# Kernel tuning notes

Hardware: AMD Instinct MI355X
Metric: run time of the kernel (lower is better)

The kernel has to match this reference:

```python
import jax, jax.numpy as jnp
import numpy as np

DIM = 2048
H = 16       # num_heads
HKV = 4      # num_kv_heads
HD = DIM // H  # head_dim = 128
REP = H // HKV
ROPE_BASE = 10000.0
QK_GAIN_INIT = 1.0
B, T = 4, 2048


def rms_norm(x):
    # F.rms_norm with eps=None -> machine eps of dtype, no weight
    eps = jnp.finfo(x.dtype).eps
    return x * jax.lax.rsqrt(jnp.mean(x * x, axis=-1, keepdims=True) + eps)


def apply_rotary_emb(x, cos, sin):
    # x: [B, h, T, HD]; cos/sin: [T, HD//2]
    h = x.shape[-1] // 2
    x1, x2 = x[..., :h], x[..., h:]
    return jnp.concatenate((x1 * cos + x2 * sin, -x1 * sin + x2 * cos), axis=-1)


def setup_inputs() -> dict:
    key = jax.random.key(0)
    ks = jax.random.split(key, 6)
    kv_dim = HKV * HD
    x = jax.random.normal(ks[0], (B, T, DIM), dtype=jnp.float32)
    Wq = jax.random.normal(ks[1], (DIM, DIM), dtype=jnp.float32) * 0.02
    Wk = jax.random.normal(ks[2], (kv_dim, DIM), dtype=jnp.float32) * 0.02
    Wv = jax.random.normal(ks[3], (kv_dim, DIM), dtype=jnp.float32) * 0.02
    Wproj = jax.random.normal(ks[4], (DIM, DIM), dtype=jnp.float32) * 0.02
    q_gain = jnp.full((H,), QK_GAIN_INIT, dtype=jnp.float32)
    return {"x": x, "Wq": Wq, "Wk": Wk, "Wv": Wv, "Wproj": Wproj, "q_gain": q_gain}


def reference(x, Wq, Wk, Wv, Wproj, q_gain):
    Bs, Ts, D = x.shape
    # QKV projections (bias-free Linear: x @ W.T)
    q = (x @ Wq.T).reshape(Bs, Ts, H, HD).transpose(0, 2, 1, 3)      # [B,H,T,HD]
    k = (x @ Wk.T).reshape(Bs, Ts, HKV, HD).transpose(0, 2, 1, 3)    # [B,HKV,T,HD]
    v = (x @ Wv.T).reshape(Bs, Ts, HKV, HD).transpose(0, 2, 1, 3)
    # RMSNorm over head_dim
    q, k = rms_norm(q), rms_norm(k)
    # rotary
    inv_freq = 1.0 / (ROPE_BASE ** (jnp.arange(0, HD, 2, dtype=jnp.float32) / HD))
    t = jnp.arange(Ts, dtype=jnp.float32)
    freqs = jnp.outer(t, inv_freq)  # [T, HD//2]
    cos, sin = jnp.cos(freqs), jnp.sin(freqs)
    q = apply_rotary_emb(q, cos, sin)
    k = apply_rotary_emb(k, cos, sin)
    # per-head query gain
    q = q * q_gain[None, :, None, None]
    # GQA attention without materializing repeated K/V
    qg = q.reshape(Bs, HKV, REP, Ts, HD)
    scale = 1.0 / jnp.sqrt(jnp.asarray(HD, dtype=q.dtype))
    scores = jnp.einsum('bgrtd,bgsd->bgrts', qg, k) * scale  # [B,HKV,REP,T,T]
    causal = jnp.tril(jnp.ones((Ts, Ts), dtype=bool))
    scores = jnp.where(causal, scores, jnp.finfo(scores.dtype).min)
    attn = jax.nn.softmax(scores, axis=-1)
    y = jnp.einsum('bgrts,bgsd->bgrtd', attn, v)              # [B,HKV,REP,T,HD]
    y = y.reshape(Bs, H, Ts, HD).transpose(0, 2, 1, 3).reshape(Bs, Ts, D)
    return y @ Wproj.T
```

## Files before the change

### kernel.cpp

```cpp
#include <hip/hip_runtime.h>
#include <stdint.h>

typedef unsigned short u16;
typedef __attribute__((ext_vector_type(4))) float f32x4;
typedef __attribute__((ext_vector_type(8))) __bf16 bf16x8;
typedef __attribute__((ext_vector_type(4))) u16 u16x4;
typedef __attribute__((ext_vector_type(8))) u16 u16x8;

#define T_SEQ 2048
#define NB 4
#define NH 16
#define NKV 4
#define HDIM 128
#define PSTR 72

__device__ __forceinline__ u16 f2bf(float f) {
  __bf16 h = (__bf16)f;
  return __builtin_bit_cast(u16, h);
}
__device__ __forceinline__ float bf2f(u16 u) {
  union { uint32_t u; float f; } v; v.u = ((uint32_t)u) << 16;
  return v.f;
}
__device__ __forceinline__ void gload16(const void* g, void* l) {
  __builtin_amdgcn_global_load_lds((const __attribute__((address_space(1))) void*)g,
                                   (__attribute__((address_space(3))) void*)l, 16, 0, 0);
}
__device__ __forceinline__ f32x4 mfma16(bf16x8 a, bf16x8 b, f32x4 c) {
  return __builtin_amdgcn_mfma_f32_16x16x32_bf16(a, b, c, 0, 0, 0);
}

__global__ __launch_bounds__(256) void cvt_bf16(const float* __restrict__ in,
                                                u16* __restrict__ out, int n) {
  int idx = blockIdx.x * 256 + threadIdx.x;
  int stride = gridDim.x * 256;
  for (int i = idx * 4; i < n; i += stride * 4) {
    f32x4 v = *(const f32x4*)(in + i);
    u16x4 o;
    o[0] = f2bf(v[0]); o[1] = f2bf(v[1]); o[2] = f2bf(v[2]); o[3] = f2bf(v[3]);
    *(u16x4*)(out + i) = o;
  }
}

template <int MODE>
__global__ __launch_bounds__(512, 2) void gemm256(const u16* __restrict__ A,
                                                  const u16* __restrict__ Bt,
                                                  u16* __restrict__ q_o, u16* __restrict__ k_o,
                                                  u16* __restrict__ v_o, float* __restrict__ f_o,
                                                  int K, int ntn, int cpx) {
  __shared__ __align__(16) u16 As[2][256 * 64];
  __shared__ __align__(16) u16 Bs[2][256 * 64];
  const int tid = threadIdx.x;
  const int l = tid & 63, w = tid >> 6;
  const int l16 = l & 15, g16 = l >> 4;
  const int wr = w >> 2, wc = w & 3;

  const int oid = blockIdx.x;
  const int wid = (oid & 7) * cpx + (oid >> 3);
  const int m0 = (wid / ntn) * 256, n0 = (wid % ntn) * 256;

  f32x4 acc[8][4] = {};

  const int srow = tid >> 3, scc = tid & 7;
  const u16* pA[4];
  const u16* pB[4];
#pragma unroll
  for (int j = 0; j < 4; ++j) {
    int row = j * 64 + srow;
    int cc = scc ^ (row & 7);
    pA[j] = A + (size_t)(m0 + row) * K + cc * 8;
    pB[j] = Bt + (size_t)(n0 + row) * K + cc * 8;
  }

#define STAGE(buf)                                              \
  {                                                             \
    char* ab = (char*)As[buf] + w * 1024;                       \
    char* bb = (char*)Bs[buf] + w * 1024;                       \
    _Pragma("unroll")                                           \
    for (int j = 0; j < 4; ++j) {                               \
      gload16(pA[j], ab + j * 8192);                            \
      pA[j] += 64;                                              \
    }                                                           \
    _Pragma("unroll")                                           \
    for (int j = 0; j < 4; ++j) {                               \
      gload16(pB[j], bb + j * 8192);                            \
      pB[j] += 64;                                              \
    }                                                           \
  }

  const int ntk = K >> 6;
  STAGE(0);
  __syncthreads();

  for (int t = 0; t < ntk; ++t) {
    const int buf = t & 1;
    if (t + 1 < ntk) STAGE(buf ^ 1);
#pragma unroll
    for (int ks = 0; ks < 2; ++ks) {
      bf16x8 bfr[4];
#pragma unroll
      for (int nf = 0; nf < 4; ++nf) {
        int brow = wc * 64 + nf * 16 + l16;
        int slot = (ks * 4 + g16) ^ (brow & 7);
        bfr[nf] = *(const bf16x8*)&Bs[buf][brow * 64 + slot * 8];
      }
#pragma unroll
      for (int rh = 0; rh < 2; ++rh) {
        bf16x8 af[4];
#pragma unroll
        for (int f = 0; f < 4; ++f) {
          int arow = wr * 128 + rh * 64 + f * 16 + l16;
          int slot = (ks * 4 + g16) ^ (arow & 7);
          af[f] = *(const bf16x8*)&As[buf][arow * 64 + slot * 8];
        }
        __builtin_amdgcn_s_setprio(1);
#pragma unroll
        for (int f = 0; f < 4; ++f)
#pragma unroll
          for (int nf = 0; nf < 4; ++nf)
            acc[rh * 4 + f][nf] = mfma16(af[f], bfr[nf], acc[rh * 4 + f][nf]);
        __builtin_amdgcn_s_setprio(0);
      }
    }
    __syncthreads();
  }
#undef STAGE

#pragma unroll
  for (int rf = 0; rf < 8; ++rf) {
#pragma unroll
    for (int rr = 0; rr < 4; ++rr) {
      int row = m0 + wr * 128 + rf * 16 + g16 * 4 + rr;
#pragma unroll
      for (int nf = 0; nf < 4; ++nf) {
        int n = n0 + wc * 64 + nf * 16 + l16;
        float val = acc[rf][nf][rr];
        if (MODE == 1) {
          f_o[(size_t)row * 2048 + n] = val;
        } else {
          int b = row >> 11, t = row & (T_SEQ - 1);
          u16 bv = f2bf(val);
          if (n < 2048) {
            int h = n >> 7, d = n & 127;
            q_o[((size_t)(b * NH + h) * T_SEQ + t) * HDIM + d] = bv;
          } else if (n < 2560) {
            int n2 = n - 2048; int h = n2 >> 7, d = n2 & 127;
            k_o[((size_t)(b * NKV + h) * T_SEQ + t) * HDIM + d] = bv;
          } else {
            int n2 = n - 2560; int h = n2 >> 7, d = n2 & 127;
            v_o[((size_t)(b * NKV + h) * T_SEQ + t) * HDIM + d] = bv;
          }
        }
      }
    }
  }
}

__global__ __launch_bounds__(256) void rmsrope(u16* __restrict__ buf,
                                               const float* __restrict__ gains,
                                               int nheads, float fold, int useGain) {
  const int w = threadIdx.x >> 6, l = threadIdx.x & 63;
  const int rid = blockIdx.x * 4 + w;
  const int t = rid & (T_SEQ - 1);
  const int h = (rid >> 11) % nheads;
  u16* p = buf + (size_t)rid * HDIM;
  float x1 = bf2f(p[l]), x2 = bf2f(p[l + 64]);
  float ss = x1 * x1 + x2 * x2;
#pragma unroll
  for (int m = 32; m; m >>= 1) ss += __shfl_xor(ss, m, 64);
  float rn = rsqrtf(ss * (1.0f / 128.0f) + 1.1920928955078125e-7f);
  float g = useGain ? gains[h] * fold : fold;
  float sc = rn * g;
  float inv = exp2f(-(float)l * (13.287712379549449f / 64.0f));
  float ang = (float)t * inv;
  float s, c;
  __sincosf(ang, &s, &c);
  float o1 = (x1 * c + x2 * s) * sc;
  float o2 = (x2 * c - x1 * s) * sc;
  p[l] = f2bf(o1);
  p[l + 64] = f2bf(o2);
}

__global__ __launch_bounds__(256) void vtrans(const u16* __restrict__ in,
                                              u16* __restrict__ out) {
  __shared__ u16 tileT[64][PSTR];
  const int tid = threadIdx.x;
  const int t0 = blockIdx.x * 64, d0 = blockIdx.y * 64, bg = blockIdx.z;
  const int row = tid >> 2, c0 = (tid & 3) * 16;
  const u16* src = in + ((size_t)bg * T_SEQ + t0 + row) * HDIM + d0 + c0;
  u16x8 a = *(const u16x8*)src;
  u16x8 bb = *(const u16x8*)(src + 8);
#pragma unroll
  for (int j = 0; j < 8; ++j) {
    tileT[c0 + j][row] = a[j];
    tileT[c0 + 8 + j][row] = bb[j];
  }
  __syncthreads();
  u16* dst = out + ((size_t)bg * HDIM + d0 + row) * T_SEQ + t0 + c0;
  *(u16x8*)dst = *(const u16x8*)&tileT[row][c0];
  *(u16x8*)(dst + 8) = *(const u16x8*)&tileT[row][c0 + 8];
}

__global__ __launch_bounds__(256) void attn_fwd3(const u16* __restrict__ qb,
                                                 const u16* __restrict__ kb,
                                                 const u16* __restrict__ vtb,
                                                 u16* __restrict__ yb,
                                                 const float* __restrict__ gains) {
  __shared__ __align__(16) u16 Ks[64 * 128];
  __shared__ __align__(16) u16 Vs[128 * 64];
  __shared__ __align__(16) u16 Ps[4][32 * PSTR];

  const int tid = threadIdx.x, l = tid & 63, w = tid >> 6;
  const int l16 = l & 15, g16 = l >> 4;

  const int oid = blockIdx.x + 8 * blockIdx.y;
  const int wid = (oid & 7) * 64 + (oid >> 3);
  const int pair = wid & 7, bh = wid >> 3;
  const int b = bh >> 4, h = bh & 15, gr = h >> 2;

  const float Mh = 16.33f * fabsf(gains[h]) + 0.5f;
  const u16* kbase = kb + (size_t)(b * NKV + gr) * T_SEQ * HDIM;
  const u16* vtbase = vtb + (size_t)(b * NKV + gr) * HDIM * T_SEQ;

  for (int phase = 0; phase < 2; ++phase) {
    const int qt = phase ? (15 - pair) : pair;
    const int q0 = qt * 128 + w * 32;
    const int qhi = q0 + 31;

    bf16x8 qf[2][4];
    const u16* qbase = qb + ((size_t)bh * T_SEQ + q0) * HDIM;
#pragma unroll
    for (int nf = 0; nf < 2; ++nf)
#pragma unroll
      for (int s = 0; s < 4; ++s)
        qf[nf][s] = *(const bf16x8*)(qbase + (size_t)(nf * 16 + l16) * HDIM + s * 32 + g16 * 8);

    f32x4 oacc[2][8] = {};
    float den[2] = {0.f, 0.f};
    const int ntile = 2 * qt + 2;

    for (int kt = 0; kt < ntile; ++kt) {
#pragma unroll
      for (int r = 0; r < 4; ++r) {
        int c = r * 256 + tid;
        int row = c >> 4, c16 = c & 15;
        int sc = c16 ^ (row & 7);
        gload16(kbase + ((size_t)(kt * 64 + row)) * HDIM + sc * 8,
                (char*)Ks + (r * 256 + w * 64) * 16);
      }
#pragma unroll
      for (int r = 0; r < 4; ++r) {
        int c = r * 256 + tid;
        int row = c >> 3, c8 = c & 7;
        int sc = c8 ^ (row & 7);
        gload16(vtbase + (size_t)row * T_SEQ + kt * 64 + sc * 8,
                (char*)Vs + (r * 256 + w * 64) * 16);
      }
      __syncthreads();

      if (kt * 64 <= qhi) {
        f32x4 sacc[4][2] = {};
        __builtin_amdgcn_s_setprio(1);
#pragma unroll
        for (int mt = 0; mt < 4; ++mt) {
          int key = mt * 16 + l16;
#pragma unroll
          for (int s = 0; s < 4; ++s) {
            bf16x8 kf = *(const bf16x8*)&Ks[key * 128 + ((s * 4 + g16) ^ (key & 7)) * 8];
#pragma unroll
            for (int nf = 0; nf < 2; ++nf)
              sacc[mt][nf] = mfma16(kf, qf[nf][s], sacc[mt][nf]);
          }
        }
        __builtin_amdgcn_s_setprio(0);

        const bool diagcross = (kt * 64 + 63 > q0);
#pragma unroll
        for (int mt = 0; mt < 4; ++mt) {
          int keyb = kt * 64 + mt * 16 + g16 * 4;
#pragma unroll
          for (int nf = 0; nf < 2; ++nf) {
            u16x4 p4;
#pragma unroll
            for (int r = 0; r < 4; ++r) {
              float pv = exp2f(sacc[mt][nf][r] - Mh);
              if (diagcross && (keyb + r > q0 + nf * 16 + l16)) pv = 0.f;
              den[nf] += pv;
              p4[r] = f2bf(pv);
            }
            *(u16x4*)&Ps[w][(nf * 16 + l16) * PSTR + mt * 16 + g16 * 4] = p4;
          }
        }

        __builtin_amdgcn_s_setprio(1);
#pragma unroll
        for (int ks = 0; ks < 2; ++ks) {
          bf16x8 pa[2];
#pragma unroll
          for (int mq = 0; mq < 2; ++mq)
            pa[mq] = *(const bf16x8*)&Ps[w][(mq * 16 + l16) * PSTR + ks * 32 + g16 * 8];
#pragma unroll
          for (int dt = 0; dt < 8; ++dt) {
            int d = dt * 16 + l16;
            bf16x8 vv = *(const bf16x8*)&Vs[d * 64 + (((ks * 4 + g16) ^ (d & 7)) * 8)];
#pragma unroll
            for (int mq = 0; mq < 2; ++mq)
              oacc[mq][dt] = mfma16(pa[mq], vv, oacc[mq][dt]);
          }
        }
        __builtin_amdgcn_s_setprio(0);
      }
      __syncthreads();
    }

#pragma unroll
    for (int nf = 0; nf < 2; ++nf) {
      den[nf] += __shfl_xor(den[nf], 16, 64);
      den[nf] += __shfl_xor(den[nf], 32, 64);
    }
    float rden[2][4];
#pragma unroll
    for (int mq = 0; mq < 2; ++mq)
#pragma unroll
      for (int r = 0; r < 4; ++r)
        rden[mq][r] = 1.f / __shfl(den[mq], g16 * 4 + r, 64);

#pragma unroll
    for (int mq = 0; mq < 2; ++mq)
#pragma unroll
      for (int dt = 0; dt < 8; ++dt)
#pragma unroll
        for (int r = 0; r < 4; ++r) {
          int t = q0 + mq * 16 + g16 * 4 + r;
          int d = dt * 16 + l16;
          yb[(((size_t)b * T_SEQ + t) * NH + h) * HDIM + d] = f2bf(oacc[mq][dt][r] * rden[mq][r]);
        }
    __syncthreads();
  }
}

extern "C" void kernel_launch(void* const* d_in, const int* in_sizes, int n_in,
                              void* d_out, int out_size, void* d_ws, size_t ws_size,
                              hipStream_t stream) {
  const float* x = (const float*)d_in[0];
  const float* Wq = (const float*)d_in[1];
  const float* Wk = (const float*)d_in[2];
  const float* Wv = (const float*)d_in[3];
  const float* Wproj = (const float*)d_in[4];
  const float* qg = (const float*)d_in[5];
  float* out = (float*)d_out;

  u16* xbf = (u16*)d_ws;
  u16* Wqkv = xbf + (size_t)8192 * 2048;
  u16* Wpj = Wqkv + (size_t)3072 * 2048;
  u16* qbuf = Wpj + (size_t)2048 * 2048;
  u16* kbuf = qbuf + (size_t)8192 * 2048;
  u16* vbuf = kbuf + (size_t)2048 * 2048;
  u16* ybuf = xbf;
  u16* vtbuf = Wqkv;

  cvt_bf16<<<8192, 256, 0, stream>>>(x, xbf, 8192 * 2048);
  cvt_bf16<<<4096, 256, 0, stream>>>(Wq, Wqkv, 2048 * 2048);
  cvt_bf16<<<1024, 256, 0, stream>>>(Wk, Wqkv + (size_t)2048 * 2048, 512 * 2048);
  cvt_bf16<<<1024, 256, 0, stream>>>(Wv, Wqkv + (size_t)2560 * 2048, 512 * 2048);
  cvt_bf16<<<4096, 256, 0, stream>>>(Wproj, Wpj, 2048 * 2048);

  gemm256<0><<<384, 512, 0, stream>>>(xbf, Wqkv, qbuf, kbuf, vbuf, nullptr, 2048, 12, 48);

  rmsrope<<<32768, 256, 0, stream>>>(qbuf, qg, NH,
                                     1.4426950408889634f / 11.313708498984761f, 1);
  rmsrope<<<8192, 256, 0, stream>>>(kbuf, nullptr, NKV, 1.0f, 0);
  vtrans<<<dim3(32, 2, 16), 256, 0, stream>>>(vbuf, vtbuf);

  attn_fwd3<<<dim3(8, 64), 256, 0, stream>>>(qbuf, kbuf, vtbuf, ybuf, qg);

  gemm256<1><<<256, 512, 0, stream>>>(ybuf, Wpj, nullptr, nullptr, nullptr, out, 2048, 8, 32);
}
```

Baseline: 378.2 us.

## Split GEMM K-tile into half-stages with finer-grained async load pipelining

```diff
diff --git a/kernel.cpp b/kernel.cpp
--- a/kernel.cpp
+++ b/kernel.cpp
@@ -43,13 +43,13 @@
 }
 
 template <int MODE>
-__global__ __launch_bounds__(512, 2) void gemm256(const u16* __restrict__ A,
-                                                  const u16* __restrict__ Bt,
-                                                  u16* __restrict__ q_o, u16* __restrict__ k_o,
-                                                  u16* __restrict__ v_o, float* __restrict__ f_o,
-                                                  int K, int ntn, int cpx) {
-  __shared__ __align__(16) u16 As[2][256 * 64];
-  __shared__ __align__(16) u16 Bs[2][256 * 64];
+__global__ __launch_bounds__(512, 2) void gemm256p4(const u16* __restrict__ A,
+                                                    const u16* __restrict__ Bt,
+                                                    u16* __restrict__ q_o, u16* __restrict__ k_o,
+                                                    u16* __restrict__ v_o, float* __restrict__ f_o,
+                                                    int K, int ntn, int cpx) {
+  __shared__ __align__(16) u16 AH[2][2][256 * 32];
+  __shared__ __align__(16) u16 BH[2][2][256 * 32];
   const int tid = threadIdx.x;
   const int l = tid & 63, w = tid >> 6;
   const int l16 = l & 15, g16 = l >> 4;
@@ -61,70 +61,88 @@
 
   f32x4 acc[8][4] = {};
 
-  const int srow = tid >> 3, scc = tid & 7;
-  const u16* pA[4];
-  const u16* pB[4];
-#pragma unroll
-  for (int j = 0; j < 4; ++j) {
-    int row = j * 64 + srow;
-    int cc = scc ^ (row & 7);
-    pA[j] = A + (size_t)(m0 + row) * K + cc * 8;
-    pB[j] = Bt + (size_t)(n0 + row) * K + cc * 8;
-  }
-
-#define STAGE(buf)                                              \
-  {                                                             \
-    char* ab = (char*)As[buf] + w * 1024;                       \
-    char* bb = (char*)Bs[buf] + w * 1024;                       \
-    _Pragma("unroll")                                           \
-    for (int j = 0; j < 4; ++j) {                               \
-      gload16(pA[j], ab + j * 8192);                            \
-      pA[j] += 64;                                              \
-    }                                                           \
-    _Pragma("unroll")                                           \
-    for (int j = 0; j < 4; ++j) {                               \
-      gload16(pB[j], bb + j * 8192);                            \
-      pB[j] += 64;                                              \
-    }                                                           \
-  }
+  const int r0 = tid >> 2, cc = tid & 3;
+  const int sc = cc ^ ((r0 >> 1) & 3);
+  const u16* pA0 = A + (size_t)(m0 + r0) * K + sc * 8;
+  const u16* pA1 = A + (size_t)(m0 + r0 + 128) * K + sc * 8;
+  const u16* pB0 = Bt + (size_t)(n0 + r0) * K + sc * 8;
+  const u16* pB1 = Bt + (size_t)(n0 + r0 + 128) * K + sc * 8;
+  const int wb = w * 1024;
+
+#define STG_A(par, kh, ko)                                        \
+  {                                                               \
+    char* d = (char*)&AH[par][kh][0] + wb;                        \
+    gload16(pA0 + (ko), d);                                       \
+    gload16(pA1 + (ko), d + 8192);                                \
+  }
+#define STG_B(par, kh, ko)                                        \
+  {                                                               \
+    char* d = (char*)&BH[par][kh][0] + wb;                        \
+    gload16(pB0 + (ko), d);                                       \
+    gload16(pB1 + (ko), d + 8192);                                \
+  }
+#define RD_B(par, kh)                                             \
+  _Pragma("unroll")                                               \
+  for (int nf = 0; nf < 4; ++nf) {                                \
+    int brow = wc * 64 + nf * 16 + l16;                           \
+    bfr[nf] = *(const bf16x8*)&BH[par][kh][brow * 32 +            \
+                               ((g16 ^ ((brow >> 1) & 3)) * 8)];  \
+  }
+#define RD_A(par, kh, rh)                                         \
+  _Pragma("unroll")                                               \
+  for (int f = 0; f < 4; ++f) {                                   \
+    int arow = wr * 128 + (rh) * 64 + f * 16 + l16;               \
+    af[f] = *(const bf16x8*)&AH[par][kh][arow * 32 +              \
+                             ((g16 ^ ((arow >> 1) & 3)) * 8)];    \
+  }
+#define MM(rh)                                                    \
+  __builtin_amdgcn_s_setprio(1);                                  \
+  _Pragma("unroll")                                               \
+  for (int f = 0; f < 4; ++f)                                     \
+    _Pragma("unroll")                                             \
+    for (int nf = 0; nf < 4; ++nf)                                \
+      acc[(rh) * 4 + f][nf] = mfma16(af[f], bfr[nf],              \
+                                     acc[(rh) * 4 + f][nf]);      \
+  __builtin_amdgcn_s_setprio(0);
 
   const int ntk = K >> 6;
-  STAGE(0);
-  __syncthreads();
+  STG_A(0, 0, 0); STG_B(0, 0, 0); STG_A(0, 1, 32); STG_B(0, 1, 32);
 
   for (int t = 0; t < ntk; ++t) {
-    const int buf = t & 1;
-    if (t + 1 < ntk) STAGE(buf ^ 1);
-#pragma unroll
-    for (int ks = 0; ks < 2; ++ks) {
-      bf16x8 bfr[4];
-#pragma unroll
-      for (int nf = 0; nf < 4; ++nf) {
-        int brow = wc * 64 + nf * 16 + l16;
-        int slot = (ks * 4 + g16) ^ (brow & 7);
-        bfr[nf] = *(const bf16x8*)&Bs[buf][brow * 64 + slot * 8];
-      }
-#pragma unroll
-      for (int rh = 0; rh < 2; ++rh) {
-        bf16x8 af[4];
-#pragma unroll
-        for (int f = 0; f < 4; ++f) {
-          int arow = wr * 128 + rh * 64 + f * 16 + l16;
-          int slot = (ks * 4 + g16) ^ (arow & 7);
-          af[f] = *(const bf16x8*)&As[buf][arow * 64 + slot * 8];
-        }
-        __builtin_amdgcn_s_setprio(1);
-#pragma unroll
-        for (int f = 0; f < 4; ++f)
-#pragma unroll
-          for (int nf = 0; nf < 4; ++nf)
-            acc[rh * 4 + f][nf] = mfma16(af[f], bfr[nf], acc[rh * 4 + f][nf]);
-        __builtin_amdgcn_s_setprio(0);
-      }
+    const int p = t & 1;
+    const bool st = (t + 1 < ntk);
+    const int ko = (t + 1) << 6;
+    bf16x8 bfr[4], af[4];
+
+    asm volatile("s_waitcnt vmcnt(4)" ::: "memory");
+    __builtin_amdgcn_s_barrier();
+    RD_B(p, 0);
+    RD_A(p, 0, 0);
+    if (st) STG_A(p ^ 1, 0, ko);
+    MM(0);
+    RD_A(p, 0, 1);
+    if (st) STG_B(p ^ 1, 0, ko);
+    MM(1);
+
+    if (st) {
+      asm volatile("s_waitcnt vmcnt(4)" ::: "memory");
+    } else {
+      asm volatile("s_waitcnt vmcnt(0)" ::: "memory");
     }
-    __syncthreads();
-  }
-#undef STAGE
+    __builtin_amdgcn_s_barrier();
+    RD_B(p, 1);
+    RD_A(p, 1, 0);
+    if (st) STG_A(p ^ 1, 1, ko + 32);
+    MM(0);
+    RD_A(p, 1, 1);
+    if (st) STG_B(p ^ 1, 1, ko + 32);
+    MM(1);
+  }
+#undef STG_A
+#undef STG_B
+#undef RD_A
+#undef RD_B
+#undef MM
 
 #pragma unroll
   for (int rf = 0; rf < 8; ++rf) {
@@ -359,13 +377,13 @@
   u16* ybuf = xbf;
   u16* vtbuf = Wqkv;
 
-  cvt_bf16<<<8192, 256, 0, stream>>>(x, xbf, 8192 * 2048);
-  cvt_bf16<<<4096, 256, 0, stream>>>(Wq, Wqkv, 2048 * 2048);
+  cvt_bf16<<<2048, 256, 0, stream>>>(x, xbf, 8192 * 2048);
+  cvt_bf16<<<2048, 256, 0, stream>>>(Wq, Wqkv, 2048 * 2048);
   cvt_bf16<<<1024, 256, 0, stream>>>(Wk, Wqkv + (size_t)2048 * 2048, 512 * 2048);
   cvt_bf16<<<1024, 256, 0, stream>>>(Wv, Wqkv + (size_t)2560 * 2048, 512 * 2048);
-  cvt_bf16<<<4096, 256, 0, stream>>>(Wproj, Wpj, 2048 * 2048);
-
-  gemm256<0><<<384, 512, 0, stream>>>(xbf, Wqkv, qbuf, kbuf, vbuf, nullptr, 2048, 12, 48);
+  cvt_bf16<<<2048, 256, 0, stream>>>(Wproj, Wpj, 2048 * 2048);
+
+  gemm256p4<0><<<384, 512, 0, stream>>>(xbf, Wqkv, qbuf, kbuf, vbuf, nullptr, 2048, 12, 48);
 
   rmsrope<<<32768, 256, 0, stream>>>(qbuf, qg, NH,
                                      1.4426950408889634f / 11.313708498984761f, 1);
@@ -374,5 +392,5 @@
 
   attn_fwd3<<<dim3(8, 64), 256, 0, stream>>>(qbuf, kbuf, vtbuf, ybuf, qg);
 
-  gemm256<1><<<256, 512, 0, stream>>>(ybuf, Wpj, nullptr, nullptr, nullptr, out, 2048, 8, 32);
-}
+  gemm256p4<1><<<256, 512, 0, stream>>>(ybuf, Wpj, nullptr, nullptr, nullptr, out, 2048, 8, 32);
+}
```

Result: faster. 363.3 us (-4.0%).
